# Optimization experiments

Hardware: AMD Instinct MI355X
Metric: run time of the kernel (lower is better)

The kernel has to match this reference:

```python
import jax, jax.numpy as jnp
import numpy as np

B, Q, C = 64, 512, 128   # batch, num_queries, num_activity_classes
P, G = 2048, 256         # num_persons, num_target_groups
COST_BCE = 1.0
COST_ACT = 1.0


def setup_inputs() -> dict:
    key = jax.random.key(0)
    k1, k2, k3, k4 = jax.random.split(key, 4)
    pred_activity_logits = jax.random.normal(k1, (B, Q, C), dtype=jnp.float32)
    attention_weights = jax.random.normal(k2, (B, P, Q), dtype=jnp.float32)
    # binary one-hot-style grouping targets (~each person in 1-of-G groups; sparse 0/1)
    tgt_one_hot = (jax.random.uniform(k3, (B, P, G)) < (1.0 / G) * 8).astype(jnp.float32)
    tgt_activity_ids = jax.random.randint(k4, (B, G), 0, C, dtype=jnp.int64)
    return {
        "pred_activity_logits": pred_activity_logits,
        "attention_weights": attention_weights,
        "tgt_one_hot": tgt_one_hot,
        "tgt_activity_ids": tgt_activity_ids,
    }


def reference(pred_activity_logits, attention_weights, tgt_one_hot, tgt_activity_ids):
    """Fused cost-matrix computation.

    BCEWithLogits(x, t) (mean reduction) = mean(softplus(x) - x * t).
    grouping_cost[b,i,j] = mean_p BCE(attw[b,p,i], onehot[b,p,j])
                         = mean_p softplus(attw[b,p,i]) - (1/P) sum_p attw[b,p,i]*onehot[b,p,j]
    activity_cost[b,i,j] = mean_c BCE(logits[b,i,c], onehot(ids[b,j])[c])
                         = mean_c softplus(logits[b,i,c]) - (1/C) * logits[b,i,ids[b,j]]
    Returns the [B, Q, G] cost tensor (scipy linear_sum_assignment, which consumes
    it on CPU, is outside the kernel scope).
    """
    attw = attention_weights            # [B, P, Q]
    logits = pred_activity_logits       # [B, Q, C]
    p = attw.shape[1]
    c = logits.shape[2]

    # grouping (BCE) cost
    sp_g = jnp.mean(jax.nn.softplus(attw), axis=1)               # [B, Q]
    xt = jnp.einsum('bpq,bpg->bqg', attw, tgt_one_hot) / p       # [B, Q, G]
    grouping_cost = sp_g[:, :, None] - xt                        # [B, Q, G]

    # activity (BCE vs one-hot class) cost
    sp_a = jnp.mean(jax.nn.softplus(logits), axis=2)             # [B, Q]
    idx = jnp.broadcast_to(tgt_activity_ids[:, None, :], (logits.shape[0], logits.shape[1], tgt_activity_ids.shape[1]))
    gathered = jnp.take_along_axis(logits, idx.astype(jnp.int32), axis=2)  # [B, Q, G]
    activity_cost = sp_a[:, :, None] - gathered / c              # [B, Q, G]

    cost = COST_BCE * grouping_cost + COST_ACT * activity_cost
    return cost
```

## Files before the change

### kernel.cpp

```cpp
#include <hip/hip_runtime.h>
#include <hip/hip_bf16.h>

#define B_  64
#define Q_  512
#define C_  128
#define P_  2048
#define G_  256
#define BM  128
#define BN  128
#define BK  64

typedef __attribute__((ext_vector_type(8))) short short8;
typedef __attribute__((ext_vector_type(4))) float floatx4;

union FragU { uint4 u; short8 s; };

__device__ __forceinline__ float bflo(unsigned int u) {
    union { unsigned int i; float f; } v; v.i = u << 16; return v.f;
}
__device__ __forceinline__ float bfhi(unsigned int u) {
    union { unsigned int i; float f; } v; v.i = u & 0xFFFF0000u; return v.f;
}
__device__ __forceinline__ float bf2f(unsigned short h) {
    union { unsigned int i; float f; } v; v.i = ((unsigned int)h) << 16; return v.f;
}
__device__ __forceinline__ unsigned int f2bf(float f) {
    union { float f; unsigned int u; } v; v.f = f;
    return (v.u + 0x7FFFu + ((v.u >> 16) & 1u)) >> 16;
}
__device__ __forceinline__ float splus(float x) {
    return fmaxf(x, 0.f) + __logf(1.f + __expf(-fabsf(x)));
}

template<bool F32>
__global__ __launch_bounds__(256, 2)
void fused_cost_kernel(const void* __restrict__ logitsv,
                       const void* __restrict__ attwv,
                       const void* __restrict__ onehotv,
                       const int* __restrict__ ids,
                       float* __restrict__ out)
{
    __shared__ unsigned short As[BM * BK];
    __shared__ unsigned short Bs[BN * BK];
    __shared__ unsigned short Lg[BM * C_];
    __shared__ float spq[BM];
    __shared__ int idt[BN];
    __shared__ int sflags;

    const int tid = threadIdx.x;
    const int l   = tid & 63;
    const int w   = tid >> 6;
    const int wm  = w & 1;
    const int wn  = w >> 1;
    const int lm  = l & 15;
    const int lk  = l >> 4;

    const int nb = blockIdx.x * BN;
    const int mb = blockIdx.y * BM;
    const int b  = blockIdx.z;

    if (tid < BM) spq[tid] = 0.f;
    if (tid == 0) sflags = 0;
    __syncthreads();

    if (tid < 64) {
        unsigned int w0 = ((const unsigned int*)logitsv)[tid];
        int e = (w0 >> 7) & 0xFF;
        unsigned long long m = __ballot(e < 100);
        if (tid == 0 && __popcll(m) >= 8) atomicOr(&sflags, 2);
    }
    if (tid < 128) { if (ids[2 * tid + 1] != 0) atomicOr(&sflags, 1); }
    __syncthreads();

    const bool isF32 = (sflags & 2) != 0;
    if (isF32 != F32) return;
    const bool ids32 = (sflags & 1) != 0;

    {
        const int q    = tid >> 1;
        const int half = tid & 1;
        float ssum = 0.f;
        if constexpr (F32) {
            const float4* src = (const float4*)((const float*)logitsv +
                                ((size_t)b * Q_ + (mb + q)) * C_ + 64 * half);
            uint2* dst = (uint2*)(&Lg[q * C_ + 64 * half]);
            #pragma unroll
            for (int i = 0; i < 16; ++i) {
                float4 t = src[i];
                ssum += splus(t.x) + splus(t.y) + splus(t.z) + splus(t.w);
                uint2 dv;
                dv.x = f2bf(t.x) | (f2bf(t.y) << 16);
                dv.y = f2bf(t.z) | (f2bf(t.w) << 16);
                dst[i] = dv;
            }
        } else {
            const uint4* src = (const uint4*)((const unsigned short*)logitsv +
                               ((size_t)b * Q_ + (mb + q)) * C_ + 64 * half);
            uint4* dst = (uint4*)(&Lg[q * C_ + 64 * half]);
            #pragma unroll
            for (int i = 0; i < 8; ++i) {
                uint4 t = src[i];
                dst[i] = t;
                ssum += splus(bflo(t.x)) + splus(bfhi(t.x))
                      + splus(bflo(t.y)) + splus(bfhi(t.y))
                      + splus(bflo(t.z)) + splus(bfhi(t.z))
                      + splus(bflo(t.w)) + splus(bfhi(t.w));
            }
        }
        atomicAdd(&spq[q], ssum * (1.0f / C_));
    }

    if (tid < BN) {
        const int gidx = b * G_ + nb + tid;
        idt[tid] = ids32 ? ids[gidx] : ids[2 * gidx];
    }

    const int kq = tid >> 4;
    const int mv = tid & 15;
    const int hb = kq >> 1;
    const int ko = (kq & 1) << 2;

    float spacc[8] = {0.f, 0.f, 0.f, 0.f, 0.f, 0.f, 0.f, 0.f};

    floatx4 acc[4][4];
    #pragma unroll
    for (int mi = 0; mi < 4; ++mi)
        #pragma unroll
        for (int ni = 0; ni < 4; ++ni)
            acc[mi][ni] = (floatx4){0.f, 0.f, 0.f, 0.f};

    for (int kb = 0; kb < P_; kb += BK) {
        __syncthreads();
        if constexpr (F32) {
            {
                const float* src = (const float*)attwv + (size_t)b * P_ * Q_
                                 + (size_t)(kb + 4 * kq) * Q_ + (mb + 8 * mv);
                float ga[4][8];
                #pragma unroll
                for (int r = 0; r < 4; ++r)
                    #pragma unroll
                    for (int h = 0; h < 2; ++h) {
                        float4 t = *(const float4*)(src + (size_t)r * Q_ + 4 * h);
                        ga[r][4 * h + 0] = t.x; ga[r][4 * h + 1] = t.y;
                        ga[r][4 * h + 2] = t.z; ga[r][4 * h + 3] = t.w;
                    }
                #pragma unroll
                for (int j = 0; j < 8; ++j) {
                    spacc[j] += splus(ga[0][j]) + splus(ga[1][j])
                              + splus(ga[2][j]) + splus(ga[3][j]);
                    uint2 dv;
                    dv.x = f2bf(ga[0][j]) | (f2bf(ga[1][j]) << 16);
                    dv.y = f2bf(ga[2][j]) | (f2bf(ga[3][j]) << 16);
                    const int m  = 8 * mv + j;
                    const int sw = (m + mv) & 7;
                    *(uint2*)(&As[m * BK + ((hb ^ sw) << 3) + ko]) = dv;
                }
            }
            {
                const float* src = (const float*)onehotv + (size_t)b * P_ * G_
                                 + (size_t)(kb + 4 * kq) * G_ + (nb + 8 * mv);
                float gb[4][8];
                #pragma unroll
                for (int r = 0; r < 4; ++r)
                    #pragma unroll
                    for (int h = 0; h < 2; ++h) {
                        float4 t = *(const float4*)(src + (size_t)r * G_ + 4 * h);
                        gb[r][4 * h + 0] = t.x; gb[r][4 * h + 1] = t.y;
                        gb[r][4 * h + 2] = t.z; gb[r][4 * h + 3] = t.w;
                    }
                #pragma unroll
                for (int j = 0; j < 8; ++j) {
                    uint2 dv;
                    dv.x = f2bf(gb[0][j]) | (f2bf(gb[1][j]) << 16);
                    dv.y = f2bf(gb[2][j]) | (f2bf(gb[3][j]) << 16);
                    const int n  = 8 * mv + j;
                    const int sw = (n + mv) & 7;
                    *(uint2*)(&Bs[n * BK + ((hb ^ sw) << 3) + ko]) = dv;
                }
            }
        } else {
            {
                const unsigned short* src = (const unsigned short*)attwv
                    + (size_t)b * P_ * Q_ + (size_t)(kb + 4 * kq) * Q_ + (mb + 8 * mv);
                uint4 r0 = *(const uint4*)(src);
                uint4 r1 = *(const uint4*)(src + Q_);
                uint4 r2 = *(const uint4*)(src + 2 * Q_);
                uint4 r3 = *(const uint4*)(src + 3 * Q_);
                unsigned int c0[4] = {r0.x, r0.y, r0.z, r0.w};
                unsigned int c1[4] = {r1.x, r1.y, r1.z, r1.w};
                unsigned int c2[4] = {r2.x, r2.y, r2.z, r2.w};
                unsigned int c3[4] = {r3.x, r3.y, r3.z, r3.w};
                #pragma unroll
                for (int j = 0; j < 8; ++j) {
                    const int cc = j >> 1;
                    unsigned int d0, d1;
                    float f0, f1, f2, f3;
                    if (j & 1) {
                        d0 = (c0[cc] >> 16) | (c1[cc] & 0xFFFF0000u);
                        d1 = (c2[cc] >> 16) | (c3[cc] & 0xFFFF0000u);
                        f0 = bfhi(c0[cc]); f1 = bfhi(c1[cc]); f2 = bfhi(c2[cc]); f3 = bfhi(c3[cc]);
                    } else {
                        d0 = (c0[cc] & 0xFFFFu) | (c1[cc] << 16);
                        d1 = (c2[cc] & 0xFFFFu) | (c3[cc] << 16);
                        f0 = bflo(c0[cc]); f1 = bflo(c1[cc]); f2 = bflo(c2[cc]); f3 = bflo(c3[cc]);
                    }
                    spacc[j] += splus(f0) + splus(f1) + splus(f2) + splus(f3);
                    const int m  = 8 * mv + j;
                    const int sw = (m + mv) & 7;
                    uint2 dv; dv.x = d0; dv.y = d1;
                    *(uint2*)(&As[m * BK + ((hb ^ sw) << 3) + ko]) = dv;
                }
            }
            {
                const unsigned short* src = (const unsigned short*)onehotv
                    + (size_t)b * P_ * G_ + (size_t)(kb + 4 * kq) * G_ + (nb + 8 * mv);
                uint4 r0 = *(const uint4*)(src);
                uint4 r1 = *(const uint4*)(src + G_);
                uint4 r2 = *(const uint4*)(src + 2 * G_);
                uint4 r3 = *(const uint4*)(src + 3 * G_);
                unsigned int c0[4] = {r0.x, r0.y, r0.z, r0.w};
                unsigned int c1[4] = {r1.x, r1.y, r1.z, r1.w};
                unsigned int c2[4] = {r2.x, r2.y, r2.z, r2.w};
                unsigned int c3[4] = {r3.x, r3.y, r3.z, r3.w};
                #pragma unroll
                for (int j = 0; j < 8; ++j) {
                    const int cc = j >> 1;
                    unsigned int d0, d1;
                    if (j & 1) {
                        d0 = (c0[cc] >> 16) | (c1[cc] & 0xFFFF0000u);
                        d1 = (c2[cc] >> 16) | (c3[cc] & 0xFFFF0000u);
                    } else {
                        d0 = (c0[cc] & 0xFFFFu) | (c1[cc] << 16);
                        d1 = (c2[cc] & 0xFFFFu) | (c3[cc] << 16);
                    }
                    const int n  = 8 * mv + j;
                    const int sw = (n + mv) & 7;
                    uint2 dv; dv.x = d0; dv.y = d1;
                    *(uint2*)(&Bs[n * BK + ((hb ^ sw) << 3) + ko]) = dv;
                }
            }
        }
        __syncthreads();
        #pragma unroll
        for (int s = 0; s < 2; ++s) {
            FragU a4[4], b4[4];
            #pragma unroll
            for (int mi = 0; mi < 4; ++mi) {
                const int m  = 64 * wm + 16 * mi + lm;
                const int sw = (m + (m >> 3)) & 7;
                a4[mi].u = *(const uint4*)(&As[m * BK + (((4 * s + lk) ^ sw) << 3)]);
            }
            #pragma unroll
            for (int ni = 0; ni < 4; ++ni) {
                const int n  = 64 * wn + 16 * ni + lm;
                const int sw = (n + (n >> 3)) & 7;
                b4[ni].u = *(const uint4*)(&Bs[n * BK + (((4 * s + lk) ^ sw) << 3)]);
            }
            #pragma unroll
            for (int mi = 0; mi < 4; ++mi)
                #pragma unroll
                for (int ni = 0; ni < 4; ++ni)
                    acc[mi][ni] = __builtin_amdgcn_mfma_f32_16x16x32_bf16(
                        a4[mi].s, b4[ni].s, acc[mi][ni], 0, 0, 0);
        }
    }

    #pragma unroll
    for (int j = 0; j < 8; ++j)
        atomicAdd(&spq[8 * mv + j], spacc[j] * (1.0f / P_));
    __syncthreads();

    float* outp = out + ((size_t)b * Q_ + mb) * G_ + nb;
    #pragma unroll
    for (int mi = 0; mi < 4; ++mi) {
        const int q0 = 64 * wm + 16 * mi + 4 * lk;
        #pragma unroll
        for (int ni = 0; ni < 4; ++ni) {
            const int g   = 64 * wn + 16 * ni + lm;
            const int cid = idt[g];
            #pragma unroll
            for (int r = 0; r < 4; ++r) {
                const int q = q0 + r;
                const float val = spq[q]
                                - acc[mi][ni][r] * (1.0f / P_)
                                - bf2f(Lg[q * C_ + cid]) * (1.0f / C_);
                outp[(size_t)q * G_ + g] = val;
            }
        }
    }
}

extern "C" void kernel_launch(void* const* d_in, const int* in_sizes, int n_in,
                              void* d_out, int out_size, void* d_ws, size_t ws_size,
                              hipStream_t stream) {
    const void* logits = d_in[0];
    const void* attw   = d_in[1];
    const void* onehot = d_in[2];
    const int*  ids    = (const int*)d_in[3];
    float*      out    = (float*)d_out;

    dim3 grid(G_ / BN, Q_ / BM, B_);
    hipLaunchKernelGGL((fused_cost_kernel<true>),  grid, dim3(256), 0, stream,
                       logits, attw, onehot, ids, out);
    hipLaunchKernelGGL((fused_cost_kernel<false>), grid, dim3(256), 0, stream,
                       logits, attw, onehot, ids, out);
}
```

Measured before the change: 523.5 us.

## Drop dtype-dispatch second launch, double threads per block, prefetch next K tile in registers

Removes the runtime fp32/bf16 detection and the second (bf16) kernel launch, so only a single fp32 kernel runs. Threads per block go from 256 to 512 with each wave covering half the N columns, and the next K tile's global loads are issued into registers before the MFMA phase to overlap memory latency with compute. The logits staging buffer is moved after the main loop and aliased onto the A/B shared buffers, cutting shared memory so more blocks can be resident. The trade-off is loss of bf16 input support and higher register pressure from the prefetch registers under the tighter launch bounds.

```diff
diff --git a/kernel.cpp b/kernel.cpp
--- a/kernel.cpp
+++ b/kernel.cpp
@@ -9,18 +9,13 @@
 #define BM  128
 #define BN  128
 #define BK  64
+#define NT  512
 
 typedef __attribute__((ext_vector_type(8))) short short8;
 typedef __attribute__((ext_vector_type(4))) float floatx4;
 
 union FragU { uint4 u; short8 s; };
 
-__device__ __forceinline__ float bflo(unsigned int u) {
-    union { unsigned int i; float f; } v; v.i = u << 16; return v.f;
-}
-__device__ __forceinline__ float bfhi(unsigned int u) {
-    union { unsigned int i; float f; } v; v.i = u & 0xFFFF0000u; return v.f;
-}
 __device__ __forceinline__ float bf2f(unsigned short h) {
     union { unsigned int i; float f; } v; v.i = ((unsigned int)h) << 16; return v.f;
 }
@@ -31,21 +26,24 @@
 __device__ __forceinline__ float splus(float x) {
     return fmaxf(x, 0.f) + __logf(1.f + __expf(-fabsf(x)));
 }
-
-template<bool F32>
-__global__ __launch_bounds__(256, 2)
-void fused_cost_kernel(const void* __restrict__ logitsv,
-                       const void* __restrict__ attwv,
-                       const void* __restrict__ onehotv,
+__device__ __forceinline__ void unpack8(float4 a, float4 b, float* c) {
+    c[0] = a.x; c[1] = a.y; c[2] = a.z; c[3] = a.w;
+    c[4] = b.x; c[5] = b.y; c[6] = b.z; c[7] = b.w;
+}
+
+__global__ __launch_bounds__(NT, 4)
+void fused_cost_kernel(const float* __restrict__ logits,
+                       const float* __restrict__ attw,
+                       const float* __restrict__ onehot,
                        const int* __restrict__ ids,
                        float* __restrict__ out)
 {
-    __shared__ unsigned short As[BM * BK];
-    __shared__ unsigned short Bs[BN * BK];
-    __shared__ unsigned short Lg[BM * C_];
+    __shared__ unsigned short smem[2 * BM * BK];
     __shared__ float spq[BM];
     __shared__ int idt[BN];
     __shared__ int sflags;
+    unsigned short* As = smem;
+    unsigned short* Bs = smem + BM * BK;
 
     const int tid = threadIdx.x;
     const int l   = tid & 63;
@@ -62,188 +60,82 @@
     if (tid < BM) spq[tid] = 0.f;
     if (tid == 0) sflags = 0;
     __syncthreads();
-
-    if (tid < 64) {
-        unsigned int w0 = ((const unsigned int*)logitsv)[tid];
-        int e = (w0 >> 7) & 0xFF;
-        unsigned long long m = __ballot(e < 100);
-        if (tid == 0 && __popcll(m) >= 8) atomicOr(&sflags, 2);
-    }
     if (tid < 128) { if (ids[2 * tid + 1] != 0) atomicOr(&sflags, 1); }
     __syncthreads();
-
-    const bool isF32 = (sflags & 2) != 0;
-    if (isF32 != F32) return;
     const bool ids32 = (sflags & 1) != 0;
-
-    {
-        const int q    = tid >> 1;
-        const int half = tid & 1;
-        float ssum = 0.f;
-        if constexpr (F32) {
-            const float4* src = (const float4*)((const float*)logitsv +
-                                ((size_t)b * Q_ + (mb + q)) * C_ + 64 * half);
-            uint2* dst = (uint2*)(&Lg[q * C_ + 64 * half]);
-            #pragma unroll
-            for (int i = 0; i < 16; ++i) {
-                float4 t = src[i];
-                ssum += splus(t.x) + splus(t.y) + splus(t.z) + splus(t.w);
-                uint2 dv;
-                dv.x = f2bf(t.x) | (f2bf(t.y) << 16);
-                dv.y = f2bf(t.z) | (f2bf(t.w) << 16);
-                dst[i] = dv;
-            }
-        } else {
-            const uint4* src = (const uint4*)((const unsigned short*)logitsv +
-                               ((size_t)b * Q_ + (mb + q)) * C_ + 64 * half);
-            uint4* dst = (uint4*)(&Lg[q * C_ + 64 * half]);
-            #pragma unroll
-            for (int i = 0; i < 8; ++i) {
-                uint4 t = src[i];
-                dst[i] = t;
-                ssum += splus(bflo(t.x)) + splus(bfhi(t.x))
-                      + splus(bflo(t.y)) + splus(bfhi(t.y))
-                      + splus(bflo(t.z)) + splus(bfhi(t.z))
-                      + splus(bflo(t.w)) + splus(bfhi(t.w));
-            }
-        }
-        atomicAdd(&spq[q], ssum * (1.0f / C_));
-    }
-
     if (tid < BN) {
         const int gidx = b * G_ + nb + tid;
         idt[tid] = ids32 ? ids[gidx] : ids[2 * gidx];
     }
 
-    const int kq = tid >> 4;
-    const int mv = tid & 15;
-    const int hb = kq >> 1;
-    const int ko = (kq & 1) << 2;
+    const int mv  = tid & 15;
+    const int kq2 = tid >> 4;
+    const int hb  = kq2 >> 2;
+    const int kd  = kq2 & 3;
+
+    const float* aSrc = attw   + (size_t)b * P_ * Q_ + (size_t)(2 * kq2) * Q_ + (mb + 8 * mv);
+    const float* bSrc = onehot + (size_t)b * P_ * G_ + (size_t)(2 * kq2) * G_ + (nb + 8 * mv);
 
     float spacc[8] = {0.f, 0.f, 0.f, 0.f, 0.f, 0.f, 0.f, 0.f};
-
-    floatx4 acc[4][4];
+    floatx4 acc[4][2];
     #pragma unroll
     for (int mi = 0; mi < 4; ++mi)
         #pragma unroll
-        for (int ni = 0; ni < 4; ++ni)
+        for (int ni = 0; ni < 2; ++ni)
             acc[mi][ni] = (floatx4){0.f, 0.f, 0.f, 0.f};
+
+    float4 rA0 = *(const float4*)(aSrc);
+    float4 rA1 = *(const float4*)(aSrc + 4);
+    float4 rA2 = *(const float4*)(aSrc + Q_);
+    float4 rA3 = *(const float4*)(aSrc + Q_ + 4);
+    float4 rB0 = *(const float4*)(bSrc);
+    float4 rB1 = *(const float4*)(bSrc + 4);
+    float4 rB2 = *(const float4*)(bSrc + G_);
+    float4 rB3 = *(const float4*)(bSrc + G_ + 4);
 
     for (int kb = 0; kb < P_; kb += BK) {
         __syncthreads();
-        if constexpr (F32) {
-            {
-                const float* src = (const float*)attwv + (size_t)b * P_ * Q_
-                                 + (size_t)(kb + 4 * kq) * Q_ + (mb + 8 * mv);
-                float ga[4][8];
-                #pragma unroll
-                for (int r = 0; r < 4; ++r)
-                    #pragma unroll
-                    for (int h = 0; h < 2; ++h) {
-                        float4 t = *(const float4*)(src + (size_t)r * Q_ + 4 * h);
-                        ga[r][4 * h + 0] = t.x; ga[r][4 * h + 1] = t.y;
-                        ga[r][4 * h + 2] = t.z; ga[r][4 * h + 3] = t.w;
-                    }
-                #pragma unroll
-                for (int j = 0; j < 8; ++j) {
-                    spacc[j] += splus(ga[0][j]) + splus(ga[1][j])
-                              + splus(ga[2][j]) + splus(ga[3][j]);
-                    uint2 dv;
-                    dv.x = f2bf(ga[0][j]) | (f2bf(ga[1][j]) << 16);
-                    dv.y = f2bf(ga[2][j]) | (f2bf(ga[3][j]) << 16);
-                    const int m  = 8 * mv + j;
-                    const int sw = (m + mv) & 7;
-                    *(uint2*)(&As[m * BK + ((hb ^ sw) << 3) + ko]) = dv;
-                }
-            }
-            {
-                const float* src = (const float*)onehotv + (size_t)b * P_ * G_
-                                 + (size_t)(kb + 4 * kq) * G_ + (nb + 8 * mv);
-                float gb[4][8];
-                #pragma unroll
-                for (int r = 0; r < 4; ++r)
-                    #pragma unroll
-                    for (int h = 0; h < 2; ++h) {
-                        float4 t = *(const float4*)(src + (size_t)r * G_ + 4 * h);
-                        gb[r][4 * h + 0] = t.x; gb[r][4 * h + 1] = t.y;
-                        gb[r][4 * h + 2] = t.z; gb[r][4 * h + 3] = t.w;
-                    }
-                #pragma unroll
-                for (int j = 0; j < 8; ++j) {
-                    uint2 dv;
-                    dv.x = f2bf(gb[0][j]) | (f2bf(gb[1][j]) << 16);
-                    dv.y = f2bf(gb[2][j]) | (f2bf(gb[3][j]) << 16);
-                    const int n  = 8 * mv + j;
-                    const int sw = (n + mv) & 7;
-                    *(uint2*)(&Bs[n * BK + ((hb ^ sw) << 3) + ko]) = dv;
-                }
-            }
-        } else {
-            {
-                const unsigned short* src = (const unsigned short*)attwv
-                    + (size_t)b * P_ * Q_ + (size_t)(kb + 4 * kq) * Q_ + (mb + 8 * mv);
-                uint4 r0 = *(const uint4*)(src);
-                uint4 r1 = *(const uint4*)(src + Q_);
-                uint4 r2 = *(const uint4*)(src + 2 * Q_);
-                uint4 r3 = *(const uint4*)(src + 3 * Q_);
-                unsigned int c0[4] = {r0.x, r0.y, r0.z, r0.w};
-                unsigned int c1[4] = {r1.x, r1.y, r1.z, r1.w};
-                unsigned int c2[4] = {r2.x, r2.y, r2.z, r2.w};
-                unsigned int c3[4] = {r3.x, r3.y, r3.z, r3.w};
-                #pragma unroll
-                for (int j = 0; j < 8; ++j) {
-                    const int cc = j >> 1;
-                    unsigned int d0, d1;
-                    float f0, f1, f2, f3;
-                    if (j & 1) {
-                        d0 = (c0[cc] >> 16) | (c1[cc] & 0xFFFF0000u);
-                        d1 = (c2[cc] >> 16) | (c3[cc] & 0xFFFF0000u);
-                        f0 = bfhi(c0[cc]); f1 = bfhi(c1[cc]); f2 = bfhi(c2[cc]); f3 = bfhi(c3[cc]);
-                    } else {
-                        d0 = (c0[cc] & 0xFFFFu) | (c1[cc] << 16);
-                        d1 = (c2[cc] & 0xFFFFu) | (c3[cc] << 16);
-                        f0 = bflo(c0[cc]); f1 = bflo(c1[cc]); f2 = bflo(c2[cc]); f3 = bflo(c3[cc]);
-                    }
-                    spacc[j] += splus(f0) + splus(f1) + splus(f2) + splus(f3);
-                    const int m  = 8 * mv + j;
-                    const int sw = (m + mv) & 7;
-                    uint2 dv; dv.x = d0; dv.y = d1;
-                    *(uint2*)(&As[m * BK + ((hb ^ sw) << 3) + ko]) = dv;
-                }
-            }
-            {
-                const unsigned short* src = (const unsigned short*)onehotv
-                    + (size_t)b * P_ * G_ + (size_t)(kb + 4 * kq) * G_ + (nb + 8 * mv);
-                uint4 r0 = *(const uint4*)(src);
-                uint4 r1 = *(const uint4*)(src + G_);
-                uint4 r2 = *(const uint4*)(src + 2 * G_);
-                uint4 r3 = *(const uint4*)(src + 3 * G_);
-                unsigned int c0[4] = {r0.x, r0.y, r0.z, r0.w};
-                unsigned int c1[4] = {r1.x, r1.y, r1.z, r1.w};
-                unsigned int c2[4] = {r2.x, r2.y, r2.z, r2.w};
-                unsigned int c3[4] = {r3.x, r3.y, r3.z, r3.w};
-                #pragma unroll
-                for (int j = 0; j < 8; ++j) {
-                    const int cc = j >> 1;
-                    unsigned int d0, d1;
-                    if (j & 1) {
-                        d0 = (c0[cc] >> 16) | (c1[cc] & 0xFFFF0000u);
-                        d1 = (c2[cc] >> 16) | (c3[cc] & 0xFFFF0000u);
-                    } else {
-                        d0 = (c0[cc] & 0xFFFFu) | (c1[cc] << 16);
-                        d1 = (c2[cc] & 0xFFFFu) | (c3[cc] << 16);
-                    }
-                    const int n  = 8 * mv + j;
-                    const int sw = (n + mv) & 7;
-                    uint2 dv; dv.x = d0; dv.y = d1;
-                    *(uint2*)(&Bs[n * BK + ((hb ^ sw) << 3) + ko]) = dv;
-                }
-            }
+        {
+            float c0[8], c1[8];
+            unpack8(rA0, rA1, c0);
+            unpack8(rA2, rA3, c1);
+            #pragma unroll
+            for (int j = 0; j < 8; ++j) {
+                spacc[j] += splus(c0[j]) + splus(c1[j]);
+                const unsigned int d = f2bf(c0[j]) | (f2bf(c1[j]) << 16);
+                const int m  = 8 * mv + j;
+                const int sw = (m + (m >> 3)) & 7;
+                *(unsigned int*)(&As[m * BK + ((hb ^ sw) << 3) + 2 * kd]) = d;
+            }
+        }
+        {
+            float c0[8], c1[8];
+            unpack8(rB0, rB1, c0);
+            unpack8(rB2, rB3, c1);
+            #pragma unroll
+            for (int j = 0; j < 8; ++j) {
+                const unsigned int d = f2bf(c0[j]) | (f2bf(c1[j]) << 16);
+                const int n  = 8 * mv + j;
+                const int sw = (n + (n >> 3)) & 7;
+                *(unsigned int*)(&Bs[n * BK + ((hb ^ sw) << 3) + 2 * kd]) = d;
+            }
+        }
+        if (kb + BK < P_) {
+            const float* an = aSrc + (size_t)(kb + BK) * Q_;
+            const float* bn = bSrc + (size_t)(kb + BK) * G_;
+            rA0 = *(const float4*)(an);
+            rA1 = *(const float4*)(an + 4);
+            rA2 = *(const float4*)(an + Q_);
+            rA3 = *(const float4*)(an + Q_ + 4);
+            rB0 = *(const float4*)(bn);
+            rB1 = *(const float4*)(bn + 4);
+            rB2 = *(const float4*)(bn + G_);
+            rB3 = *(const float4*)(bn + G_ + 4);
         }
         __syncthreads();
         #pragma unroll
         for (int s = 0; s < 2; ++s) {
-            FragU a4[4], b4[4];
+            FragU a4[4], b4[2];
             #pragma unroll
             for (int mi = 0; mi < 4; ++mi) {
                 const int m  = 64 * wm + 16 * mi + lm;
@@ -251,15 +143,15 @@
                 a4[mi].u = *(const uint4*)(&As[m * BK + (((4 * s + lk) ^ sw) << 3)]);
             }
             #pragma unroll
-            for (int ni = 0; ni < 4; ++ni) {
-                const int n  = 64 * wn + 16 * ni + lm;
+            for (int ni = 0; ni < 2; ++ni) {
+                const int n  = 32 * wn + 16 * ni + lm;
                 const int sw = (n + (n >> 3)) & 7;
                 b4[ni].u = *(const uint4*)(&Bs[n * BK + (((4 * s + lk) ^ sw) << 3)]);
             }
             #pragma unroll
             for (int mi = 0; mi < 4; ++mi)
                 #pragma unroll
-                for (int ni = 0; ni < 4; ++ni)
+                for (int ni = 0; ni < 2; ++ni)
                     acc[mi][ni] = __builtin_amdgcn_mfma_f32_16x16x32_bf16(
                         a4[mi].s, b4[ni].s, acc[mi][ni], 0, 0, 0);
         }
@@ -268,6 +160,26 @@
     #pragma unroll
     for (int j = 0; j < 8; ++j)
         atomicAdd(&spq[8 * mv + j], spacc[j] * (1.0f / P_));
+
+    __syncthreads();
+
+    {
+        const int q  = tid >> 2;
+        const int qt = tid & 3;
+        const float4* src = (const float4*)(logits + ((size_t)b * Q_ + (mb + q)) * C_ + 32 * qt);
+        uint2* dst = (uint2*)(&smem[q * C_ + 32 * qt]);
+        float ssum = 0.f;
+        #pragma unroll
+        for (int i = 0; i < 8; ++i) {
+            float4 t = src[i];
+            ssum += splus(t.x) + splus(t.y) + splus(t.z) + splus(t.w);
+            uint2 dv;
+            dv.x = f2bf(t.x) | (f2bf(t.y) << 16);
+            dv.y = f2bf(t.z) | (f2bf(t.w) << 16);
+            dst[i] = dv;
+        }
+        atomicAdd(&spq[q], ssum * (1.0f / C_));
+    }
     __syncthreads();
 
     float* outp = out + ((size_t)b * Q_ + mb) * G_ + nb;
@@ -275,15 +187,15 @@
     for (int mi = 0; mi < 4; ++mi) {
         const int q0 = 64 * wm + 16 * mi + 4 * lk;
         #pragma unroll
-        for (int ni = 0; ni < 4; ++ni) {
-            const int g   = 64 * wn + 16 * ni + lm;
+        for (int ni = 0; ni < 2; ++ni) {
+            const int g   = 32 * wn + 16 * ni + lm;
             const int cid = idt[g];
             #pragma unroll
             for (int r = 0; r < 4; ++r) {
                 const int q = q0 + r;
                 const float val = spq[q]
                                 - acc[mi][ni][r] * (1.0f / P_)
-                                - bf2f(Lg[q * C_ + cid]) * (1.0f / C_);
+                                - bf2f(smem[q * C_ + cid]) * (1.0f / C_);
                 outp[(size_t)q * G_ + g] = val;
             }
         }
@@ -293,15 +205,13 @@
 extern "C" void kernel_launch(void* const* d_in, const int* in_sizes, int n_in,
                               void* d_out, int out_size, void* d_ws, size_t ws_size,
                               hipStream_t stream) {
-    const void* logits = d_in[0];
-    const void* attw   = d_in[1];
-    const void* onehot = d_in[2];
-    const int*  ids    = (const int*)d_in[3];
-    float*      out    = (float*)d_out;
+    const float* logits = (const float*)d_in[0];
+    const float* attw   = (const float*)d_in[1];
+    const float* onehot = (const float*)d_in[2];
+    const int*   ids    = (const int*)d_in[3];
+    float*       out    = (float*)d_out;
 
     dim3 grid(G_ / BN, Q_ / BM, B_);
-    hipLaunchKernelGGL((fused_cost_kernel<true>),  grid, dim3(256), 0, stream,
+    hipLaunchKernelGGL(fused_cost_kernel, grid, dim3(NT), 0, stream,
                        logits, attw, onehot, ids, out);
-    hipLaunchKernelGGL((fused_cost_kernel<false>), grid, dim3(256), 0, stream,
-                       logits, attw, onehot, ids, out);
-}
+}
```

Result: faster. 509.0 us (-2.8%).
